# Kernel optimization log

Measured on AMD Instinct MI355X. Metric: run time of the kernel, lower is better.

The kernel has to match this reference:

```python
import jax, jax.numpy as jnp
import numpy as np

N_NODES = 50000
N_EDGES = 800000
H_DIM = 128


def setup_inputs() -> dict:
    key = jax.random.key(0)
    ks = jax.random.split(key, 12)
    h = jax.random.normal(ks[0], (N_NODES, H_DIM), dtype=jnp.float32)
    feat_ct = jax.random.normal(ks[1], (N_EDGES, 1), dtype=jnp.float32)
    feat_cb = jax.random.normal(ks[2], (N_EDGES, 1), dtype=jnp.float32)
    src_ct = jax.random.randint(ks[3], (N_EDGES,), 0, N_NODES, dtype=jnp.int32)
    dst_ct = jax.random.randint(ks[4], (N_EDGES,), 0, N_NODES, dtype=jnp.int32)
    src_cb = jax.random.randint(ks[5], (N_EDGES,), 0, N_NODES, dtype=jnp.int32)
    dst_cb = jax.random.randint(ks[6], (N_EDGES,), 0, N_NODES, dtype=jnp.int32)
    # torch Linear(2h, h): weight [h, 2h]; store transposed [2h, h], kaiming-ish scale
    scale = 1.0 / np.sqrt(2 * H_DIM)
    W0 = jax.random.uniform(ks[7], (2 * H_DIM, H_DIM), minval=-scale, maxval=scale, dtype=jnp.float32)
    b0 = jnp.zeros((H_DIM,), dtype=jnp.float32)
    W1 = jax.random.uniform(ks[8], (2 * H_DIM, H_DIM), minval=-scale, maxval=scale, dtype=jnp.float32)
    b1 = jnp.zeros((H_DIM,), dtype=jnp.float32)
    return {"h": h, "feat_ct": feat_ct, "feat_cb": feat_cb,
            "src_ct": src_ct, "dst_ct": dst_ct, "src_cb": src_cb, "dst_cb": dst_cb,
            "W0": W0, "b0": b0, "W1": W1, "b1": b1}


def _agg(h, feat, src, dst, n):
    # e_mul_u: per-edge scalar weight * source node feature, sum-reduced to dst
    return jax.ops.segment_sum(feat * h[src], dst, num_segments=n)


def reference(h, feat_ct, feat_cb, src_ct, dst_ct, src_cb, dst_cb, W0, b0, W1, b1):
    n = h.shape[0]
    for W, b in ((W0, b0), (W1, b1)):
        m_ct = _agg(h, feat_ct, src_ct, dst_ct, n)   # [N, h]
        m_cb = _agg(h, feat_cb, src_cb, dst_cb, n)   # [N, h]
        t = jnp.concatenate([m_ct, m_cb], axis=-1)   # [N, 2h]
        h_ = jax.nn.gelu(t @ W + b, approximate=False)
        h = h + h_                                    # residual update of node 'h'
    return h
```

## Files before the change

kernel.cpp:

```cpp
#include <hip/hip_runtime.h>
#include <math.h>

#define HDIM 128
#define CH 4096
typedef unsigned int uint;
using short8 = __attribute__((ext_vector_type(8))) short;
using f32x4  = __attribute__((ext_vector_type(4))) float;

__device__ __forceinline__ uint pack_bf16x2(float a, float b) {
    uint ua = __float_as_uint(a), ub = __float_as_uint(b);
    ua = (ua + 0x7fffu + ((ua >> 16) & 1u)) >> 16;
    ub = (ub + 0x7fffu + ((ub >> 16) & 1u)) & 0xffff0000u;
    return ua | ub;
}
__device__ __forceinline__ unsigned short pack_bf16(float a) {
    uint ua = __float_as_uint(a);
    return (unsigned short)((ua + 0x7fffu + ((ua >> 16) & 1u)) >> 16);
}

__global__ __launch_bounds__(256) void prep_hist_kernel(
    const float* __restrict__ h, uint* __restrict__ hb, int n_pairs,
    const float* __restrict__ W0, const float* __restrict__ W1,
    unsigned short* __restrict__ Wt0, unsigned short* __restrict__ Wt1,
    int conv_blocks,
    const int* __restrict__ dst_ct, int* __restrict__ cntm_ct, int n_ct, int nv_ct,
    const int* __restrict__ dst_cb, int* __restrict__ cntm_cb, int n_cb, int nv_cb,
    int nbuckets)
{
    if ((int)blockIdx.x < conv_blocks) {
        const int total = n_pairs + 2 * 32768;
        for (int i = blockIdx.x * 256 + threadIdx.x; i < total;
             i += conv_blocks * 256) {
            if (i < n_pairs) {
                float2 v = reinterpret_cast<const float2*>(h)[i];
                hb[i] = pack_bf16x2(v.x, v.y);
            } else {
                int t = i - n_pairs;
                const float* W = (t < 32768) ? W0 : W1;
                unsigned short* Wt = (t < 32768) ? Wt0 : Wt1;
                int j = t & 32767;
                int c = j >> 8, k = j & 255;
                Wt[j] = pack_bf16(W[k * HDIM + c]);
            }
        }
        return;
    }
    __shared__ int lh[512];
    const int hb_id = blockIdx.x - conv_blocks;
    const bool cb = (hb_id >= nv_ct);
    const int vb = cb ? hb_id - nv_ct : hb_id;
    const int* dst = cb ? dst_cb : dst_ct;
    int* cntm      = cb ? cntm_cb : cntm_ct;
    const int n  = cb ? n_cb : n_ct;
    const int NV = cb ? nv_cb : nv_ct;
    for (int j = threadIdx.x; j < 512; j += 256) lh[j] = 0;
    __syncthreads();
    const int e0 = vb << 12;
    const int e1 = min(n, e0 + CH);
    for (int i = e0 + threadIdx.x; i < e1; i += 256)
        atomicAdd(&lh[dst[i] >> 7], 1);
    __syncthreads();
    for (int j = threadIdx.x; j < nbuckets; j += 256)
        cntm[j * NV + vb] = lh[j];
}

__global__ __launch_bounds__(256) void scanA_kernel(
    int* __restrict__ cntm_ct, int* __restrict__ tot_ct, int nv_ct,
    int* __restrict__ cntm_cb, int* __restrict__ tot_cb, int nv_cb,
    int nbuckets)
{
    __shared__ int buf[256];
    const bool cb = ((int)blockIdx.x >= nbuckets);
    const int b = cb ? blockIdx.x - nbuckets : blockIdx.x;
    int* cntm = cb ? cntm_cb : cntm_ct;
    int* tot  = cb ? tot_cb : tot_ct;
    const int NV = cb ? nv_cb : nv_ct;
    const int t = threadIdx.x;
    int base = 0;
    for (int t0 = 0; t0 < NV; t0 += 256) {
        const int idx = t0 + t;
        const int v = (idx < NV) ? cntm[b * NV + idx] : 0;
        buf[t] = v;
        __syncthreads();
        #pragma unroll
        for (int off = 1; off < 256; off <<= 1) {
            int x = (t >= off) ? buf[t - off] : 0;
            __syncthreads();
            buf[t] += x;
            __syncthreads();
        }
        if (idx < NV) cntm[b * NV + idx] = base + buf[t] - v;
        base += buf[255];
        __syncthreads();
    }
    if (t == 0) tot[b] = base;
}

__global__ __launch_bounds__(1024) void scanB_kernel(
    const int* __restrict__ tot_ct, int* __restrict__ bkt_ct,
    const int* __restrict__ tot_cb, int* __restrict__ bkt_cb, int nbuckets)
{
    __shared__ int buf[1024];
    const int* tot = blockIdx.x ? tot_cb : tot_ct;
    int* bkt       = blockIdx.x ? bkt_cb : bkt_ct;
    const int t = threadIdx.x;
    const int v = (t < nbuckets) ? tot[t] : 0;
    buf[t] = v;
    __syncthreads();
    #pragma unroll
    for (int off = 1; off < 1024; off <<= 1) {
        int x = (t >= off) ? buf[t - off] : 0;
        __syncthreads();
        buf[t] += x;
        __syncthreads();
    }
    if (t < nbuckets) bkt[t] = buf[t] - v;
    if (t == nbuckets - 1) bkt[nbuckets] = buf[t];
}

__global__ __launch_bounds__(256) void part_kernel(
    const int* __restrict__ dst_ct, const int* __restrict__ src_ct,
    const float* __restrict__ feat_ct, const int* __restrict__ off_ct,
    const int* __restrict__ bkt_ct, int2* __restrict__ ebkt_ct, int n_ct, int nv_ct,
    const int* __restrict__ dst_cb, const int* __restrict__ src_cb,
    const float* __restrict__ feat_cb, const int* __restrict__ off_cb,
    const int* __restrict__ bkt_cb, int2* __restrict__ ebkt_cb, int n_cb, int nv_cb,
    int nbuckets)
{
    __shared__ int cur[512];
    const bool cb = ((int)blockIdx.x >= nv_ct);
    const int vb = cb ? blockIdx.x - nv_ct : blockIdx.x;
    const int* dst    = cb ? dst_cb : dst_ct;
    const int* srcp   = cb ? src_cb : src_ct;
    const float* feat = cb ? feat_cb : feat_ct;
    const int* off    = cb ? off_cb : off_ct;
    const int* bkt    = cb ? bkt_cb : bkt_ct;
    int2* ebkt        = cb ? ebkt_cb : ebkt_ct;
    const int n  = cb ? n_cb : n_ct;
    const int NV = cb ? nv_cb : nv_ct;
    for (int j = threadIdx.x; j < nbuckets; j += 256)
        cur[j] = off[j * NV + vb] + bkt[j];
    __syncthreads();
    const int e0 = vb << 12;
    const int e1 = min(n, e0 + CH);
    for (int i = e0 + threadIdx.x; i < e1; i += 256) {
        int d = dst[i];
        int p = atomicAdd(&cur[d >> 7], 1);
        ebkt[p] = make_int2((srcp[i] & 0xFFFF) | ((d & 127) << 16),
                            __float_as_int(feat[i]));
    }
}

__global__ __launch_bounds__(256) void sortb_kernel(
    const int2* __restrict__ ebkt_ct, const int* __restrict__ bkt_ct,
    const int2* __restrict__ ebkt_cb, const int* __restrict__ bkt_cb,
    uint* __restrict__ ecsr_ct, uint* __restrict__ ecsr_cb,
    int* __restrict__ rowptr_ct, int* __restrict__ rowptr_cb,
    int n_nodes, int nbuckets)
{
    __shared__ int cnt[128];
    __shared__ int pref[128];
    const int b = blockIdx.x >> 1;
    const bool cb = blockIdx.x & 1;
    const int2* ebkt = cb ? ebkt_cb : ebkt_ct;
    const int* bkt   = cb ? bkt_cb : bkt_ct;
    uint* ecsr       = cb ? ecsr_cb : ecsr_ct;
    int* rowptr      = cb ? rowptr_cb : rowptr_ct;
    const int t = threadIdx.x;
    const int beg = bkt[b], end = bkt[b + 1];

    if (t < 128) cnt[t] = 0;
    __syncthreads();
    for (int i = beg + t; i < end; i += 256)
        atomicAdd(&cnt[((uint)ebkt[i].x) >> 16], 1);
    __syncthreads();
    if (t < 128) pref[t] = cnt[t];
    __syncthreads();
    #pragma unroll
    for (int off = 1; off < 128; off <<= 1) {
        int v = 0;
        if (t < 128 && t >= off) v = pref[t - off];
        __syncthreads();
        if (t < 128) pref[t] += v;
        __syncthreads();
    }
    if (t < 128) {
        int n0 = b * 128;
        int base = beg + pref[t] - cnt[t];
        if (n0 + t < n_nodes) rowptr[n0 + t] = base;
        cnt[t] = base;
    }
    if (b == nbuckets - 1 && t == 0) rowptr[n_nodes] = end;
    __syncthreads();
    for (int i = beg + t; i < end; i += 256) {
        int2 r = ebkt[i];
        int d = ((uint)r.x) >> 16;
        int p = atomicAdd(&cnt[d], 1);
        ecsr[p] = (uint)(r.x & 0xFFFF) |
                  ((uint)pack_bf16(__int_as_float(r.y)) << 16);
    }
}

__global__ __launch_bounds__(256) void csr_gather_bf16_kernel(
    const uint4* __restrict__ hb,
    const int* __restrict__ rp_ct, const uint* __restrict__ e_ct,
    const int* __restrict__ rp_cb, const uint* __restrict__ e_cb,
    uint4* __restrict__ mct, uint4* __restrict__ mcb, int n_nodes)
{
    const int lane = threadIdx.x & 63;
    const int eg = lane >> 4;
    const int q  = lane & 15;
    const int wave = (blockIdx.x * 256 + threadIdx.x) >> 6;
    const int nwaves = (gridDim.x * 256) >> 6;
    const int total = 2 * n_nodes;
    for (int v = wave; v < total; v += nwaves) {
        const bool cbt = (v >= n_nodes);
        const int n = cbt ? (v - n_nodes) : v;
        const int* rp    = cbt ? rp_cb : rp_ct;
        const uint* ecsr = cbt ? e_cb : e_ct;
        uint4* m = cbt ? mcb : mct;
        const int beg = rp[n], end = rp[n + 1];
        float a0 = 0.f, a1 = 0.f, a2 = 0.f, a3 = 0.f;
        float a4 = 0.f, a5 = 0.f, a6 = 0.f, a7 = 0.f;
        for (int i0 = beg; i0 < end; i0 += 64) {
            const int cnt = min(64, end - i0);
            uint e = 0;
            if (lane < cnt) e = ecsr[i0 + lane];
            const int nquad = (cnt + 3) >> 2;
            #pragma unroll 4
            for (int jj = 0; jj < nquad; ++jj) {
                uint ej = __shfl(e, jj * 4 + eg);
                int   sj = (int)(ej & 0xFFFFu);
                float fj = __uint_as_float(ej & 0xffff0000u);
                uint4 hv = hb[(size_t)sj * 16 + q];
                a0 = fmaf(fj, __uint_as_float(hv.x << 16),         a0);
                a1 = fmaf(fj, __uint_as_float(hv.x & 0xffff0000u), a1);
                a2 = fmaf(fj, __uint_as_float(hv.y << 16),         a2);
                a3 = fmaf(fj, __uint_as_float(hv.y & 0xffff0000u), a3);
                a4 = fmaf(fj, __uint_as_float(hv.z << 16),         a4);
                a5 = fmaf(fj, __uint_as_float(hv.z & 0xffff0000u), a5);
                a6 = fmaf(fj, __uint_as_float(hv.w << 16),         a6);
                a7 = fmaf(fj, __uint_as_float(hv.w & 0xffff0000u), a7);
            }
        }
        a0 += __shfl_xor(a0, 16); a1 += __shfl_xor(a1, 16);
        a2 += __shfl_xor(a2, 16); a3 += __shfl_xor(a3, 16);
        a4 += __shfl_xor(a4, 16); a5 += __shfl_xor(a5, 16);
        a6 += __shfl_xor(a6, 16); a7 += __shfl_xor(a7, 16);
        a0 += __shfl_xor(a0, 32); a1 += __shfl_xor(a1, 32);
        a2 += __shfl_xor(a2, 32); a3 += __shfl_xor(a3, 32);
        a4 += __shfl_xor(a4, 32); a5 += __shfl_xor(a5, 32);
        a6 += __shfl_xor(a6, 32); a7 += __shfl_xor(a7, 32);
        if (eg == 0) {
            uint4 o;
            o.x = pack_bf16x2(a0, a1);
            o.y = pack_bf16x2(a2, a3);
            o.z = pack_bf16x2(a4, a5);
            o.w = pack_bf16x2(a6, a7);
            m[(size_t)n * 16 + q] = o;
        }
    }
}

__global__ __launch_bounds__(256) void gemm_mfma_kernel(
    const unsigned short* __restrict__ mct, const unsigned short* __restrict__ mcb,
    const unsigned short* __restrict__ Wt, const float* __restrict__ bias,
    const float* __restrict__ h_in, const unsigned short* __restrict__ hb_in,
    float* __restrict__ h_out, unsigned short* __restrict__ hb_out,
    int n_nodes, int mode)
{
    const int base = blockIdx.x * 128;
    const int lane = threadIdx.x & 63;
    const int wid  = threadIdx.x >> 6;
    const int lr = lane & 15, lg = lane >> 4;
    const int row0 = base + wid * 32;

    f32x4 acc[2][8];
    #pragma unroll
    for (int mi = 0; mi < 2; ++mi)
        #pragma unroll
        for (int ni = 0; ni < 8; ++ni)
            acc[mi][ni] = (f32x4){0.f, 0.f, 0.f, 0.f};

    const int last = (base + 128 > n_nodes);

    #pragma unroll
    for (int ks = 0; ks < 8; ++ks) {
        const int koff = ks * 32 + lg * 8;
        short8 a[2], b[8];
        #pragma unroll
        for (int mi = 0; mi < 2; ++mi) {
            int node = row0 + mi * 16 + lr;
            if (last && node >= n_nodes) node = n_nodes - 1;
            const unsigned short* srcp = (koff < 128)
                ? (mct + (size_t)node * HDIM + koff)
                : (mcb + (size_t)node * HDIM + (koff - 128));
            a[mi] = *reinterpret_cast<const short8*>(srcp);
        }
        #pragma unroll
        for (int ni = 0; ni < 8; ++ni) {
            int col = ni * 16 + lr;
            b[ni] = *reinterpret_cast<const short8*>(Wt + (size_t)col * 256 + koff);
        }
        #pragma unroll
        for (int mi = 0; mi < 2; ++mi)
            #pragma unroll
            for (int ni = 0; ni < 8; ++ni)
                acc[mi][ni] = __builtin_amdgcn_mfma_f32_16x16x32_bf16(
                    a[mi], b[ni], acc[mi][ni], 0, 0, 0);
    }

    #pragma unroll
    for (int mi = 0; mi < 2; ++mi) {
        #pragma unroll
        for (int ni = 0; ni < 8; ++ni) {
            const int col = ni * 16 + lr;
            const float bc = bias[col];
            #pragma unroll
            for (int j = 0; j < 4; ++j) {
                int node = row0 + mi * 16 + lg * 4 + j;
                if (node < n_nodes) {
                    float x = acc[mi][ni][j] + bc;
                    float g = 0.5f * x * (1.0f + erff(x * 0.70710678118654752f));
                    const size_t idx = (size_t)node * HDIM + col;
                    if (mode == 0) {
                        float o = h_in[idx] + g;
                        hb_out[idx] = pack_bf16(o);
                    } else {
                        float hprev = __uint_as_float((uint)hb_in[idx] << 16);
                        h_out[idx] = hprev + g;
                    }
                }
            }
        }
    }
}

__global__ __launch_bounds__(256) void edge_agg_kernel(
    const float* __restrict__ h, const float* __restrict__ feat,
    const int* __restrict__ src, const int* __restrict__ dst,
    float* __restrict__ m, int n_edges)
{
    long long tid = (long long)blockIdx.x * 256 + threadIdx.x;
    int e = (int)(tid >> 5);
    if (e >= n_edges) return;
    int q = (int)(tid & 31);
    float f = feat[e];
    size_t s = (size_t)src[e] * HDIM;
    size_t d = (size_t)dst[e] * HDIM;
    float4 v = reinterpret_cast<const float4*>(h + s)[q];
    float* mp = m + d + (size_t)q * 4;
    unsafeAtomicAdd(mp + 0, f * v.x);
    unsafeAtomicAdd(mp + 1, f * v.y);
    unsafeAtomicAdd(mp + 2, f * v.z);
    unsafeAtomicAdd(mp + 3, f * v.w);
}

__global__ __launch_bounds__(256) void gemm_gelu_res_kernel(
    const float* __restrict__ mct, const float* __restrict__ mcb,
    const float* __restrict__ W, const float* __restrict__ bias,
    const float* __restrict__ h_in, float* __restrict__ h_out, int n_nodes)
{
    __shared__ float Wl[256 * HDIM];
    __shared__ float trow[8][2 * HDIM];
    for (int i = threadIdx.x; i < 256 * HDIM; i += 256)
        Wl[i] = W[i];
    const int c = threadIdx.x & 127;
    const int g = threadIdx.x >> 7;
    const float bc = bias[c];
    __syncthreads();
    const int niter = (n_nodes + 7) >> 3;
    for (int it = blockIdx.x; it < niter; it += gridDim.x) {
        __syncthreads();
        for (int j = threadIdx.x; j < 8 * 256; j += 256) {
            int nn = j >> 8;
            int k  = j & 255;
            long long node = (long long)it * 8 + nn;
            float val = 0.0f;
            if (node < n_nodes)
                val = (k < HDIM) ? mct[node * HDIM + k]
                                 : mcb[node * HDIM + (k - HDIM)];
            trow[nn][k] = val;
        }
        __syncthreads();
        const float* t0 = trow[g * 4 + 0];
        const float* t1 = trow[g * 4 + 1];
        const float* t2 = trow[g * 4 + 2];
        const float* t3 = trow[g * 4 + 3];
        float a0 = bc, a1 = bc, a2 = bc, a3 = bc;
        #pragma unroll 8
        for (int k = 0; k < 256; ++k) {
            float w = Wl[k * HDIM + c];
            a0 = fmaf(t0[k], w, a0);
            a1 = fmaf(t1[k], w, a1);
            a2 = fmaf(t2[k], w, a2);
            a3 = fmaf(t3[k], w, a3);
        }
        float accs[4] = {a0, a1, a2, a3};
        #pragma unroll
        for (int j = 0; j < 4; ++j) {
            long long node = (long long)it * 8 + g * 4 + j;
            if (node < n_nodes) {
                float x = accs[j];
                float gl = 0.5f * x * (1.0f + erff(x * 0.70710678118654752f));
                h_out[node * HDIM + c] = h_in[node * HDIM + c] + gl;
            }
        }
    }
}

extern "C" void kernel_launch(void* const* d_in, const int* in_sizes, int n_in,
                              void* d_out, int out_size, void* d_ws, size_t ws_size,
                              hipStream_t stream)
{
    const float* h0      = (const float*)d_in[0];
    const float* feat_ct = (const float*)d_in[1];
    const float* feat_cb = (const float*)d_in[2];
    const int*   src_ct  = (const int*)d_in[3];
    const int*   dst_ct  = (const int*)d_in[4];
    const int*   src_cb  = (const int*)d_in[5];
    const int*   dst_cb  = (const int*)d_in[6];
    const float* W0      = (const float*)d_in[7];
    const float* b0      = (const float*)d_in[8];
    const float* W1      = (const float*)d_in[9];
    const float* b1      = (const float*)d_in[10];

    const int n_nodes    = in_sizes[0] / HDIM;
    const int n_edges_ct = in_sizes[3];
    const int n_edges_cb = in_sizes[5];
    float* out = (float*)d_out;

    const int nbuckets = (n_nodes + 127) >> 7;
    const int nv_ct = (n_edges_ct + CH - 1) / CH;
    const int nv_cb = (n_edges_cb + CH - 1) / CH;

    char* p = (char*)d_ws;
    auto take = [&](size_t bytes) -> char* {
        char* r = p;
        p += (bytes + 255) & ~(size_t)255;
        return r;
    };
    unsigned short* hb   = (unsigned short*)take((size_t)n_nodes * HDIM * 2);
    unsigned short* mctb = (unsigned short*)take((size_t)n_nodes * HDIM * 2);
    unsigned short* mcbb = (unsigned short*)take((size_t)n_nodes * HDIM * 2);
    unsigned short* Wt0  = (unsigned short*)take(32768 * 2);
    unsigned short* Wt1  = (unsigned short*)take(32768 * 2);
    int* cntm_ct = (int*)take((size_t)nbuckets * nv_ct * 4);
    int* cntm_cb = (int*)take((size_t)nbuckets * nv_cb * 4);
    int* tot_ct  = (int*)take((size_t)nbuckets * 4);
    int* tot_cb  = (int*)take((size_t)nbuckets * 4);
    int* bkt_ct  = (int*)take(((size_t)nbuckets + 1) * 4);
    int* bkt_cb  = (int*)take(((size_t)nbuckets + 1) * 4);
    int* rowptr_ct = (int*)take(((size_t)n_nodes + 1) * 4);
    int* rowptr_cb = (int*)take(((size_t)n_nodes + 1) * 4);
    uint* ecsr_ct = (uint*)take((size_t)n_edges_ct * 4);
    uint* ecsr_cb = (uint*)take((size_t)n_edges_cb * 4);
    const size_t need_bytes = (size_t)(p - (char*)d_ws);
    int2* ebkt_ct = (int2*)mctb;
    int2* ebkt_cb = (int2*)mcbb;

    const bool ebkt_fits =
        ((size_t)n_edges_ct * 8 <= (size_t)n_nodes * HDIM * 2) &&
        ((size_t)n_edges_cb * 8 <= (size_t)n_nodes * HDIM * 2);

    if (ws_size >= need_bytes && n_nodes <= 65536 && ebkt_fits) {
        const int conv_blocks = 2048;
        prep_hist_kernel<<<conv_blocks + nv_ct + nv_cb, 256, 0, stream>>>(
            h0, (uint*)hb, n_nodes * (HDIM / 2), W0, W1, Wt0, Wt1, conv_blocks,
            dst_ct, cntm_ct, n_edges_ct, nv_ct,
            dst_cb, cntm_cb, n_edges_cb, nv_cb, nbuckets);
        scanA_kernel<<<nbuckets * 2, 256, 0, stream>>>(
            cntm_ct, tot_ct, nv_ct, cntm_cb, tot_cb, nv_cb, nbuckets);
        scanB_kernel<<<2, 1024, 0, stream>>>(
            tot_ct, bkt_ct, tot_cb, bkt_cb, nbuckets);
        part_kernel<<<nv_ct + nv_cb, 256, 0, stream>>>(
            dst_ct, src_ct, feat_ct, cntm_ct, bkt_ct, ebkt_ct, n_edges_ct, nv_ct,
            dst_cb, src_cb, feat_cb, cntm_cb, bkt_cb, ebkt_cb, n_edges_cb, nv_cb,
            nbuckets);
        sortb_kernel<<<nbuckets * 2, 256, 0, stream>>>(
            ebkt_ct, bkt_ct, ebkt_cb, bkt_cb, ecsr_ct, ecsr_cb,
            rowptr_ct, rowptr_cb, n_nodes, nbuckets);
        const int gemm_blocks = (n_nodes + 127) / 128;
        csr_gather_bf16_kernel<<<2048, 256, 0, stream>>>(
            (const uint4*)hb, rowptr_ct, ecsr_ct, rowptr_cb, ecsr_cb,
            (uint4*)mctb, (uint4*)mcbb, n_nodes);
        gemm_mfma_kernel<<<gemm_blocks, 256, 0, stream>>>(
            mctb, mcbb, Wt0, b0, h0, hb, out, hb, n_nodes, 0);
        csr_gather_bf16_kernel<<<2048, 256, 0, stream>>>(
            (const uint4*)hb, rowptr_ct, ecsr_ct, rowptr_cb, ecsr_cb,
            (uint4*)mctb, (uint4*)mcbb, n_nodes);
        gemm_mfma_kernel<<<gemm_blocks, 256, 0, stream>>>(
            mctb, mcbb, Wt1, b1, h0, hb, out, hb, n_nodes, 1);
    } else {
        float* mct = (float*)d_ws;
        float* mcb = mct + (size_t)n_nodes * HDIM;
        const size_t mbytes = (size_t)n_nodes * HDIM * sizeof(float) * 2;
        const int agg_blocks_ct = (int)(((long long)n_edges_ct * 32 + 255) / 256);
        const int agg_blocks_cb = (int)(((long long)n_edges_cb * 32 + 255) / 256);
        const float* hcur = h0;
        for (int layer = 0; layer < 2; ++layer) {
            hipMemsetAsync(d_ws, 0, mbytes, stream);
            edge_agg_kernel<<<agg_blocks_ct, 256, 0, stream>>>(
                hcur, feat_ct, src_ct, dst_ct, mct, n_edges_ct);
            edge_agg_kernel<<<agg_blocks_cb, 256, 0, stream>>>(
                hcur, feat_cb, src_cb, dst_cb, mcb, n_edges_cb);
            gemm_gelu_res_kernel<<<256, 256, 0, stream>>>(
                mct, mcb, layer ? W1 : W0, layer ? b1 : b0, hcur, out, n_nodes);
            hcur = out;
        }
    }
}
```

Before: 259.6 us.

## Map one node per 16-lane group in gather, stage sort buckets in LDS

```diff
diff --git a/kernel.cpp b/kernel.cpp
--- a/kernel.cpp
+++ b/kernel.cpp
@@ -2,7 +2,8 @@
 #include <math.h>
 
 #define HDIM 128
-#define CH 4096
+#define CH 8192
+#define SORTB_CAP 4096
 typedef unsigned int uint;
 using short8 = __attribute__((ext_vector_type(8))) short;
 using f32x4  = __attribute__((ext_vector_type(4))) float;
@@ -55,7 +56,7 @@
     const int NV = cb ? nv_cb : nv_ct;
     for (int j = threadIdx.x; j < 512; j += 256) lh[j] = 0;
     __syncthreads();
-    const int e0 = vb << 12;
+    const int e0 = vb * CH;
     const int e1 = min(n, e0 + CH);
     for (int i = e0 + threadIdx.x; i < e1; i += 256)
         atomicAdd(&lh[dst[i] >> 7], 1);
@@ -141,7 +142,7 @@
     for (int j = threadIdx.x; j < nbuckets; j += 256)
         cur[j] = off[j * NV + vb] + bkt[j];
     __syncthreads();
-    const int e0 = vb << 12;
+    const int e0 = vb * CH;
     const int e1 = min(n, e0 + CH);
     for (int i = e0 + threadIdx.x; i < e1; i += 256) {
         int d = dst[i];
@@ -160,6 +161,7 @@
 {
     __shared__ int cnt[128];
     __shared__ int pref[128];
+    __shared__ int2 rec[SORTB_CAP];
     const int b = blockIdx.x >> 1;
     const bool cb = blockIdx.x & 1;
     const int2* ebkt = cb ? ebkt_cb : ebkt_ct;
@@ -168,11 +170,21 @@
     int* rowptr      = cb ? rowptr_cb : rowptr_ct;
     const int t = threadIdx.x;
     const int beg = bkt[b], end = bkt[b + 1];
+    const int span = end - beg;
+    const bool stage = (span <= SORTB_CAP);
 
     if (t < 128) cnt[t] = 0;
     __syncthreads();
-    for (int i = beg + t; i < end; i += 256)
-        atomicAdd(&cnt[((uint)ebkt[i].x) >> 16], 1);
+    if (stage) {
+        for (int i = t; i < span; i += 256) {
+            int2 r = ebkt[beg + i];
+            rec[i] = r;
+            atomicAdd(&cnt[((uint)r.x) >> 16], 1);
+        }
+    } else {
+        for (int i = beg + t; i < end; i += 256)
+            atomicAdd(&cnt[((uint)ebkt[i].x) >> 16], 1);
+    }
     __syncthreads();
     if (t < 128) pref[t] = cnt[t];
     __syncthreads();
@@ -192,12 +204,22 @@
     }
     if (b == nbuckets - 1 && t == 0) rowptr[n_nodes] = end;
     __syncthreads();
-    for (int i = beg + t; i < end; i += 256) {
-        int2 r = ebkt[i];
-        int d = ((uint)r.x) >> 16;
-        int p = atomicAdd(&cnt[d], 1);
-        ecsr[p] = (uint)(r.x & 0xFFFF) |
-                  ((uint)pack_bf16(__int_as_float(r.y)) << 16);
+    if (stage) {
+        for (int i = t; i < span; i += 256) {
+            int2 r = rec[i];
+            int d = ((uint)r.x) >> 16;
+            int p = atomicAdd(&cnt[d], 1);
+            ecsr[p] = (uint)(r.x & 0xFFFF) |
+                      ((uint)pack_bf16(__int_as_float(r.y)) << 16);
+        }
+    } else {
+        for (int i = beg + t; i < end; i += 256) {
+            int2 r = ebkt[i];
+            int d = ((uint)r.x) >> 16;
+            int p = atomicAdd(&cnt[d], 1);
+            ecsr[p] = (uint)(r.x & 0xFFFF) |
+                      ((uint)pack_bf16(__int_as_float(r.y)) << 16);
+        }
     }
 }
 
@@ -210,10 +232,10 @@
     const int lane = threadIdx.x & 63;
     const int eg = lane >> 4;
     const int q  = lane & 15;
-    const int wave = (blockIdx.x * 256 + threadIdx.x) >> 6;
-    const int nwaves = (gridDim.x * 256) >> 6;
+    const int grp = (((blockIdx.x * 256 + threadIdx.x) >> 6) << 2) + eg;
+    const int ngrp = ((gridDim.x * 256) >> 6) << 2;
     const int total = 2 * n_nodes;
-    for (int v = wave; v < total; v += nwaves) {
+    for (int v = grp; v < total; v += ngrp) {
         const bool cbt = (v >= n_nodes);
         const int n = cbt ? (v - n_nodes) : v;
         const int* rp    = cbt ? rp_cb : rp_ct;
@@ -222,43 +244,27 @@
         const int beg = rp[n], end = rp[n + 1];
         float a0 = 0.f, a1 = 0.f, a2 = 0.f, a3 = 0.f;
         float a4 = 0.f, a5 = 0.f, a6 = 0.f, a7 = 0.f;
-        for (int i0 = beg; i0 < end; i0 += 64) {
-            const int cnt = min(64, end - i0);
-            uint e = 0;
-            if (lane < cnt) e = ecsr[i0 + lane];
-            const int nquad = (cnt + 3) >> 2;
-            #pragma unroll 4
-            for (int jj = 0; jj < nquad; ++jj) {
-                uint ej = __shfl(e, jj * 4 + eg);
-                int   sj = (int)(ej & 0xFFFFu);
-                float fj = __uint_as_float(ej & 0xffff0000u);
-                uint4 hv = hb[(size_t)sj * 16 + q];
-                a0 = fmaf(fj, __uint_as_float(hv.x << 16),         a0);
-                a1 = fmaf(fj, __uint_as_float(hv.x & 0xffff0000u), a1);
-                a2 = fmaf(fj, __uint_as_float(hv.y << 16),         a2);
-                a3 = fmaf(fj, __uint_as_float(hv.y & 0xffff0000u), a3);
-                a4 = fmaf(fj, __uint_as_float(hv.z << 16),         a4);
-                a5 = fmaf(fj, __uint_as_float(hv.z & 0xffff0000u), a5);
-                a6 = fmaf(fj, __uint_as_float(hv.w << 16),         a6);
-                a7 = fmaf(fj, __uint_as_float(hv.w & 0xffff0000u), a7);
-            }
-        }
-        a0 += __shfl_xor(a0, 16); a1 += __shfl_xor(a1, 16);
-        a2 += __shfl_xor(a2, 16); a3 += __shfl_xor(a3, 16);
-        a4 += __shfl_xor(a4, 16); a5 += __shfl_xor(a5, 16);
-        a6 += __shfl_xor(a6, 16); a7 += __shfl_xor(a7, 16);
-        a0 += __shfl_xor(a0, 32); a1 += __shfl_xor(a1, 32);
-        a2 += __shfl_xor(a2, 32); a3 += __shfl_xor(a3, 32);
-        a4 += __shfl_xor(a4, 32); a5 += __shfl_xor(a5, 32);
-        a6 += __shfl_xor(a6, 32); a7 += __shfl_xor(a7, 32);
-        if (eg == 0) {
-            uint4 o;
-            o.x = pack_bf16x2(a0, a1);
-            o.y = pack_bf16x2(a2, a3);
-            o.z = pack_bf16x2(a4, a5);
-            o.w = pack_bf16x2(a6, a7);
-            m[(size_t)n * 16 + q] = o;
-        }
+        #pragma unroll 4
+        for (int i = beg; i < end; ++i) {
+            uint ej = ecsr[i];
+            int   sj = (int)(ej & 0xFFFFu);
+            float fj = __uint_as_float(ej & 0xffff0000u);
+            uint4 hv = hb[(size_t)sj * 16 + q];
+            a0 = fmaf(fj, __uint_as_float(hv.x << 16),         a0);
+            a1 = fmaf(fj, __uint_as_float(hv.x & 0xffff0000u), a1);
+            a2 = fmaf(fj, __uint_as_float(hv.y << 16),         a2);
+            a3 = fmaf(fj, __uint_as_float(hv.y & 0xffff0000u), a3);
+            a4 = fmaf(fj, __uint_as_float(hv.z << 16),         a4);
+            a5 = fmaf(fj, __uint_as_float(hv.z & 0xffff0000u), a5);
+            a6 = fmaf(fj, __uint_as_float(hv.w << 16),         a6);
+            a7 = fmaf(fj, __uint_as_float(hv.w & 0xffff0000u), a7);
+        }
+        uint4 o;
+        o.x = pack_bf16x2(a0, a1);
+        o.y = pack_bf16x2(a2, a3);
+        o.z = pack_bf16x2(a4, a5);
+        o.w = pack_bf16x2(a6, a7);
+        m[(size_t)n * 16 + q] = o;
     }
 }
 
```

Result: slower. 279.4 us (+7.6%).
